# Kernel tuning notes

Hardware: AMD Instinct MI355X
Metric: run time of the kernel (lower is better)

The kernel has to match this reference:

```python
import jax, jax.numpy as jnp
import numpy as np

NUM_RADIAL = 6
HIDDEN = 128
OUT_EMB = 256
OUT_CH = 128
NUM_LAYERS = 3
E = 1600000
N_NODES = 50000


def setup_inputs() -> dict:
    key = jax.random.key(0)
    ks = jax.random.split(key, 16)
    inp = {
        "x": jax.random.normal(ks[0], (E, HIDDEN), dtype=jnp.float32),
        "rbf": jax.random.normal(ks[1], (E, NUM_RADIAL), dtype=jnp.float32),
        "idx_i": jax.random.randint(ks[2], (E,), 0, N_NODES, dtype=jnp.int32),
        "num_nodes": N_NODES,
        # torch nn.Linear weights are [out, in]
        "W_basis": jax.random.normal(ks[3], (HIDDEN, NUM_RADIAL), dtype=jnp.float32) * 0.3,
        "W_proj": jax.random.normal(ks[4], (OUT_EMB, HIDDEN), dtype=jnp.float32) * 0.08,
        "W_final": jax.random.normal(ks[5], (OUT_CH, OUT_EMB), dtype=jnp.float32) * 0.06,
    }
    for l in range(NUM_LAYERS):
        inp[f"W{l}"] = jax.random.normal(ks[6 + 2 * l], (OUT_EMB, OUT_EMB), dtype=jnp.float32) * 0.06
        inp[f"b{l}"] = jnp.zeros((OUT_EMB,), dtype=jnp.float32)
    return inp


def reference(x, rbf, idx_i, num_nodes, W_basis, W_proj, W_final, W0, b0, W1, b1, W2, b2):
    # basis_transformation: [E, num_radial] -> [E, hidden]
    basis = rbf @ W_basis.T
    # elementwise mul then edge->node scatter-sum
    msg = basis * x                                  # [E, hidden]
    agg = jax.ops.segment_sum(msg, idx_i, num_segments=num_nodes)  # [N, hidden]
    # output_projection (no bias)
    h = agg @ W_proj.T                                # [N, out_emb]
    for W, b in ((W0, b0), (W1, b1), (W2, b2)):
        h = jax.nn.silu(h @ W.T + b)
    return h @ W_final.T                              # [N, out_channels]
```

## Files before the change

### kernel.cpp

```cpp
#include <hip/hip_runtime.h>

typedef float f4 __attribute__((ext_vector_type(4)));
typedef float f2 __attribute__((ext_vector_type(2)));
typedef short bf16x8 __attribute__((ext_vector_type(8)));
typedef unsigned short u16x8 __attribute__((ext_vector_type(8)));
typedef unsigned short u16x4 __attribute__((ext_vector_type(4)));
typedef float f32x4 __attribute__((ext_vector_type(4)));

constexpr int HIDDEN     = 128;
constexpr int OUT_EMB    = 256;
constexpr int OUT_CH     = 128;
constexpr int NUM_RADIAL = 6;
constexpr int NBLK       = 64;

constexpr int OFF_Wp = 0;
constexpr int OFF_W0 = OFF_Wp + 256 * 128;
constexpr int OFF_W1 = OFF_W0 + 256 * 256;
constexpr int OFF_W2 = OFF_W1 + 256 * 256;
constexpr int OFF_Wf = OFF_W2 + 256 * 256;
constexpr int WTOT   = OFF_Wf + 128 * 256;

__device__ __forceinline__ unsigned short f2bf(float f) {
    unsigned int u = __float_as_uint(f);
    return (unsigned short)((u + 0x7FFFu + ((u >> 16) & 1u)) >> 16);
}
__device__ __forceinline__ float bf2f(unsigned short h) {
    return __uint_as_float(((unsigned int)h) << 16);
}

__global__ __launch_bounds__(256) void prep_kernel(
    const float* __restrict__ Wp, const float* __restrict__ W0,
    const float* __restrict__ W1, const float* __restrict__ W2,
    const float* __restrict__ Wf,
    unsigned short* __restrict__ whi, unsigned short* __restrict__ wlo,
    int* __restrict__ count, int N)
{
    const int i = blockIdx.x * 256 + threadIdx.x;
    if (i < N) count[i] = 0;
    if (i < WTOT) {
        const float* src; int off;
        if      (i < OFF_W0) { src = Wp; off = i - OFF_Wp; }
        else if (i < OFF_W1) { src = W0; off = i - OFF_W0; }
        else if (i < OFF_W2) { src = W1; off = i - OFF_W1; }
        else if (i < OFF_Wf) { src = W2; off = i - OFF_W2; }
        else                 { src = Wf; off = i - OFF_Wf; }
        float v = src[off];
        unsigned short h = f2bf(v);
        whi[i] = h;
        wlo[i] = f2bf(v - bf2f(h));
    }
}

__global__ __launch_bounds__(256) void hist_kernel(const int* __restrict__ idx,
                                                   int* __restrict__ count, long E)
{
    long i = (long)blockIdx.x * blockDim.x + threadIdx.x;
    if (i < E) atomicAdd(&count[idx[i]], 1);
}

__global__ __launch_bounds__(1024) void scan_kernel(const int* __restrict__ count,
                                                    int* __restrict__ start,
                                                    int* __restrict__ cursor, int N)
{
    __shared__ int part[1024];
    const int tid   = threadIdx.x;
    const int chunk = (N + 1023) / 1024;
    const int lo    = tid * chunk;
    const int hi    = min(lo + chunk, N);

    int s = 0;
    for (int i = lo; i < hi; ++i) s += count[i];
    part[tid] = s;
    __syncthreads();

    for (int off = 1; off < 1024; off <<= 1) {
        int v = part[tid];
        int u = (tid >= off) ? part[tid - off] : 0;
        __syncthreads();
        part[tid] = v + u;
        __syncthreads();
    }

    int run = (tid > 0) ? part[tid - 1] : 0;
    for (int i = lo; i < hi; ++i) {
        start[i]  = run;
        cursor[i] = run;
        run += count[i];
    }
    if (tid == 1023) start[N] = part[1023];
}

__global__ __launch_bounds__(256) void scatter_perm_kernel(const int* __restrict__ idx,
                                                           int* __restrict__ cursor,
                                                           int* __restrict__ perm, long E)
{
    long i = (long)blockIdx.x * blockDim.x + threadIdx.x;
    if (i < E) {
        int p = atomicAdd(&cursor[idx[i]], 1);
        perm[p] = (int)i;
    }
}

__device__ __forceinline__ void edge_accum(const float* __restrict__ x,
                                           const float* __restrict__ rbf,
                                           const float wb[4][NUM_RADIAL],
                                           int e, int l, f4& acc)
{
    const float* rp = rbf + (long)e * NUM_RADIAL;
    f2 r01 = *(const f2*)(rp);
    f2 r23 = *(const f2*)(rp + 2);
    f2 r45 = *(const f2*)(rp + 4);
    f4 xv  = *(const f4*)(x + (long)e * HIDDEN + 4 * l);
    float rb[NUM_RADIAL] = {r01[0], r01[1], r23[0], r23[1], r45[0], r45[1]};
#pragma unroll
    for (int c = 0; c < 4; ++c) {
        float b = 0.f;
#pragma unroll
        for (int r = 0; r < NUM_RADIAL; ++r) b = __builtin_fmaf(rb[r], wb[c][r], b);
        acc[c] = __builtin_fmaf(b, xv[c], acc[c]);
    }
}

__global__ __launch_bounds__(256) void gather_kernel(
    const float* __restrict__ x, const float* __restrict__ rbf,
    const float* __restrict__ Wb, const int* __restrict__ perm,
    const int* __restrict__ start, unsigned short* __restrict__ aggb, int N)
{
    const int lane = threadIdx.x & 63;
    const int half = lane >> 5;
    const int l    = lane & 31;
    const int wid  = threadIdx.x >> 6;
    const int node = blockIdx.x * 4 + wid;
    if (node >= N) return;

    float wb[4][NUM_RADIAL];
#pragma unroll
    for (int c = 0; c < 4; ++c)
#pragma unroll
        for (int r = 0; r < NUM_RADIAL; ++r)
            wb[c][r] = Wb[(4 * l + c) * NUM_RADIAL + r];

    const int j0 = start[node], j1 = start[node + 1];
    f4 acc = {0.f, 0.f, 0.f, 0.f};

    int j = j0 + half;
    for (; j + 2 < j1; j += 4) {
        const int ea = perm[j];
        const int eb = perm[j + 2];
        edge_accum(x, rbf, wb, ea, l, acc);
        edge_accum(x, rbf, wb, eb, l, acc);
    }
    if (j < j1) edge_accum(x, rbf, wb, perm[j], l, acc);

#pragma unroll
    for (int c = 0; c < 4; ++c) acc[c] += __shfl_xor(acc[c], 32);

    if (half == 0) {
        u16x4 o;
#pragma unroll
        for (int c = 0; c < 4; ++c) o[c] = f2bf(acc[c]);
        *(u16x4*)(aggb + (long)node * HIDDEN + 4 * l) = o;
    }
}

__device__ __forceinline__ int swz(int node, int col) {
    return (node * 256 + col) ^ ((node & 7) << 3);
}

template <int IN, int OUT, bool BIAS_ACT, bool LAST>
__device__ __forceinline__ void mfma_layer(
    const unsigned short* __restrict__ whi, const unsigned short* __restrict__ wlo,
    const float* __restrict__ bias,
    unsigned short* H, float* __restrict__ outp,
    int node0, int N, int w, int lane)
{
    const int lr = lane & 15;
    const int lg = lane >> 4;
    constexpr int NT = OUT / 64;
    const int wbase = w * (OUT / 4);

    f32x4 acc[4][NT];
#pragma unroll
    for (int nt = 0; nt < NT; ++nt) {
        float bb = 0.f;
        if constexpr (BIAS_ACT) bb = bias[wbase + nt * 16 + lr];
#pragma unroll
        for (int mt = 0; mt < 4; ++mt) {
            acc[mt][nt][0] = bb; acc[mt][nt][1] = bb;
            acc[mt][nt][2] = bb; acc[mt][nt][3] = bb;
        }
    }

    for (int ks = 0; ks < IN / 32; ++ks) {
        const int k0 = ks * 32 + lg * 8;
        bf16x8 ah[4];
#pragma unroll
        for (int mt = 0; mt < 4; ++mt) {
            const int node = mt * 16 + lr;
            ah[mt] = *(const bf16x8*)&H[swz(node, k0)];
        }
#pragma unroll
        for (int nt = 0; nt < NT; ++nt) {
            const long wrow = (long)(wbase + nt * 16 + lr) * IN + k0;
            bf16x8 bh = *(const bf16x8*)&whi[wrow];
            bf16x8 bl = *(const bf16x8*)&wlo[wrow];
#pragma unroll
            for (int mt = 0; mt < 4; ++mt) {
                acc[mt][nt] = __builtin_amdgcn_mfma_f32_16x16x32_bf16(ah[mt], bh, acc[mt][nt], 0, 0, 0);
                acc[mt][nt] = __builtin_amdgcn_mfma_f32_16x16x32_bf16(ah[mt], bl, acc[mt][nt], 0, 0, 0);
            }
        }
    }

    __syncthreads();

#pragma unroll
    for (int mt = 0; mt < 4; ++mt) {
#pragma unroll
        for (int nt = 0; nt < NT; ++nt) {
#pragma unroll
            for (int r = 0; r < 4; ++r) {
                float v = acc[mt][nt][r];
                if constexpr (BIAS_ACT) v = v / (1.f + __expf(-v));
                const int node = mt * 16 + lg * 4 + r;
                const int col  = wbase + nt * 16 + lr;
                if constexpr (LAST) {
                    if (node0 + node < N) outp[(long)(node0 + node) * OUT + col] = v;
                } else {
                    H[swz(node, col)] = f2bf(v);
                }
            }
        }
    }
    if constexpr (!LAST) __syncthreads();
}

__global__ __launch_bounds__(256, 3) void node_mlp_mfma_kernel(
    const unsigned short* __restrict__ aggb,
    const unsigned short* __restrict__ whi, const unsigned short* __restrict__ wlo,
    const float* __restrict__ b0, const float* __restrict__ b1,
    const float* __restrict__ b2,
    float* __restrict__ out, int N)
{
    __shared__ unsigned short H[NBLK * 256];

    const int tid   = threadIdx.x;
    const int w     = tid >> 6;
    const int lane  = tid & 63;
    const int node0 = blockIdx.x * NBLK;

#pragma unroll
    for (int i = 0; i < (NBLK * HIDDEN) / (256 * 8); ++i) {
        const int e    = (i * 256 + tid) * 8;
        const int node = e >> 7;
        const int col  = e & 127;
        u16x8 v = {0, 0, 0, 0, 0, 0, 0, 0};
        if (node0 + node < N) v = *(const u16x8*)(aggb + (long)(node0 + node) * HIDDEN + col);
        *(u16x8*)&H[swz(node, col)] = v;
    }
    __syncthreads();

    mfma_layer<HIDDEN,  OUT_EMB, false, false>(whi + OFF_Wp, wlo + OFF_Wp, nullptr, H, nullptr, node0, N, w, lane);
    mfma_layer<OUT_EMB, OUT_EMB, true,  false>(whi + OFF_W0, wlo + OFF_W0, b0,      H, nullptr, node0, N, w, lane);
    mfma_layer<OUT_EMB, OUT_EMB, true,  false>(whi + OFF_W1, wlo + OFF_W1, b1,      H, nullptr, node0, N, w, lane);
    mfma_layer<OUT_EMB, OUT_EMB, true,  false>(whi + OFF_W2, wlo + OFF_W2, b2,      H, nullptr, node0, N, w, lane);
    mfma_layer<OUT_EMB, OUT_CH,  false, true >(whi + OFF_Wf, wlo + OFF_Wf, nullptr, H, out,     node0, N, w, lane);
}

extern "C" void kernel_launch(void* const* d_in, const int* in_sizes, int n_in,
                              void* d_out, int out_size, void* d_ws, size_t ws_size,
                              hipStream_t stream)
{
    const float* x   = (const float*)d_in[0];
    const float* rbf = (const float*)d_in[1];
    const int*   idx = (const int*)d_in[2];
    const float* Wb  = (const float*)d_in[4];
    const float* Wp  = (const float*)d_in[5];
    const float* Wf  = (const float*)d_in[6];
    const float* W0  = (const float*)d_in[7];
    const float* b0  = (const float*)d_in[8];
    const float* W1  = (const float*)d_in[9];
    const float* b1  = (const float*)d_in[10];
    const float* W2  = (const float*)d_in[11];
    const float* b2  = (const float*)d_in[12];

    const long E = (long)in_sizes[0] / HIDDEN;
    const int  N = out_size / OUT_CH;

    unsigned short* aggb = (unsigned short*)d_ws;
    int* count  = (int*)(aggb + (long)N * HIDDEN);
    int* startp = count + N;
    int* cursor = startp + N + 1;
    int* perm   = cursor + N;
    uintptr_t p = (uintptr_t)(perm + E);
    p = (p + 15) & ~(uintptr_t)15;
    unsigned short* whi = (unsigned short*)p;
    unsigned short* wlo = whi + WTOT;

    const int pb = (max((int)WTOT, N) + 255) / 256;
    prep_kernel<<<pb, 256, 0, stream>>>(Wp, W0, W1, W2, Wf, whi, wlo, count, N);

    const int eb = (int)((E + 255) / 256);
    hist_kernel<<<eb, 256, 0, stream>>>(idx, count, E);
    scan_kernel<<<1, 1024, 0, stream>>>(count, startp, cursor, N);
    scatter_perm_kernel<<<eb, 256, 0, stream>>>(idx, cursor, perm, E);
    gather_kernel<<<(N + 3) / 4, 256, 0, stream>>>(x, rbf, Wb, perm, startp, aggb, N);

    node_mlp_mfma_kernel<<<(N + NBLK - 1) / NBLK, 256, 0, stream>>>(
        aggb, whi, wlo, b0, b1, b2, (float*)d_out, N);
}
```

Measured before the change: 719.2 us.

## Fuse edge gather into node MLP kernel and vectorize histogram/scatter

Removes the separate gather kernel and its bf16 aggregate buffer. Each MLP block now gathers its own 64 nodes, with each wave walking 16 nodes in turn, and writes the aggregated rows straight into shared memory before the MFMA layers. The histogram and permutation-scatter kernels also load four indices per thread with one vector load. This drops a kernel launch and a global round trip. The cost is far fewer concurrent waves for the latency-bound irregular gather, and the occupancy hint on the MLP kernel is gone.

```diff
diff --git a/kernel.cpp b/kernel.cpp
--- a/kernel.cpp
+++ b/kernel.cpp
@@ -2,6 +2,7 @@
 
 typedef float f4 __attribute__((ext_vector_type(4)));
 typedef float f2 __attribute__((ext_vector_type(2)));
+typedef int   i4 __attribute__((ext_vector_type(4)));
 typedef short bf16x8 __attribute__((ext_vector_type(8)));
 typedef unsigned short u16x8 __attribute__((ext_vector_type(8)));
 typedef unsigned short u16x4 __attribute__((ext_vector_type(4)));
@@ -54,8 +55,14 @@
 __global__ __launch_bounds__(256) void hist_kernel(const int* __restrict__ idx,
                                                    int* __restrict__ count, long E)
 {
-    long i = (long)blockIdx.x * blockDim.x + threadIdx.x;
-    if (i < E) atomicAdd(&count[idx[i]], 1);
+    long i = ((long)blockIdx.x * blockDim.x + threadIdx.x) * 4;
+    if (i + 3 < E) {
+        i4 v = *(const i4*)(idx + i);
+#pragma unroll
+        for (int k = 0; k < 4; ++k) atomicAdd(&count[v[k]], 1);
+    } else {
+        for (long t = i; t < E; ++t) atomicAdd(&count[idx[t]], 1);
+    }
 }
 
 __global__ __launch_bounds__(1024) void scan_kernel(const int* __restrict__ count,
@@ -94,11 +101,24 @@
                                                            int* __restrict__ cursor,
                                                            int* __restrict__ perm, long E)
 {
-    long i = (long)blockIdx.x * blockDim.x + threadIdx.x;
-    if (i < E) {
-        int p = atomicAdd(&cursor[idx[i]], 1);
-        perm[p] = (int)i;
-    }
+    long i = ((long)blockIdx.x * blockDim.x + threadIdx.x) * 4;
+    if (i + 3 < E) {
+        i4 v = *(const i4*)(idx + i);
+#pragma unroll
+        for (int k = 0; k < 4; ++k) {
+            int p = atomicAdd(&cursor[v[k]], 1);
+            perm[p] = (int)(i + k);
+        }
+    } else {
+        for (long t = i; t < E; ++t) {
+            int p = atomicAdd(&cursor[idx[t]], 1);
+            perm[p] = (int)t;
+        }
+    }
+}
+
+__device__ __forceinline__ int swz(int node, int col) {
+    return (node * 256 + col) ^ ((node & 7) << 3);
 }
 
 __device__ __forceinline__ void edge_accum(const float* __restrict__ x,
@@ -119,52 +139,6 @@
         for (int r = 0; r < NUM_RADIAL; ++r) b = __builtin_fmaf(rb[r], wb[c][r], b);
         acc[c] = __builtin_fmaf(b, xv[c], acc[c]);
     }
-}
-
-__global__ __launch_bounds__(256) void gather_kernel(
-    const float* __restrict__ x, const float* __restrict__ rbf,
-    const float* __restrict__ Wb, const int* __restrict__ perm,
-    const int* __restrict__ start, unsigned short* __restrict__ aggb, int N)
-{
-    const int lane = threadIdx.x & 63;
-    const int half = lane >> 5;
-    const int l    = lane & 31;
-    const int wid  = threadIdx.x >> 6;
-    const int node = blockIdx.x * 4 + wid;
-    if (node >= N) return;
-
-    float wb[4][NUM_RADIAL];
-#pragma unroll
-    for (int c = 0; c < 4; ++c)
-#pragma unroll
-        for (int r = 0; r < NUM_RADIAL; ++r)
-            wb[c][r] = Wb[(4 * l + c) * NUM_RADIAL + r];
-
-    const int j0 = start[node], j1 = start[node + 1];
-    f4 acc = {0.f, 0.f, 0.f, 0.f};
-
-    int j = j0 + half;
-    for (; j + 2 < j1; j += 4) {
-        const int ea = perm[j];
-        const int eb = perm[j + 2];
-        edge_accum(x, rbf, wb, ea, l, acc);
-        edge_accum(x, rbf, wb, eb, l, acc);
-    }
-    if (j < j1) edge_accum(x, rbf, wb, perm[j], l, acc);
-
-#pragma unroll
-    for (int c = 0; c < 4; ++c) acc[c] += __shfl_xor(acc[c], 32);
-
-    if (half == 0) {
-        u16x4 o;
-#pragma unroll
-        for (int c = 0; c < 4; ++c) o[c] = f2bf(acc[c]);
-        *(u16x4*)(aggb + (long)node * HIDDEN + 4 * l) = o;
-    }
-}
-
-__device__ __forceinline__ int swz(int node, int col) {
-    return (node * 256 + col) ^ ((node & 7) << 3);
 }
 
 template <int IN, int OUT, bool BIAS_ACT, bool LAST>
@@ -235,8 +209,10 @@
     if constexpr (!LAST) __syncthreads();
 }
 
-__global__ __launch_bounds__(256, 3) void node_mlp_mfma_kernel(
-    const unsigned short* __restrict__ aggb,
+__global__ __launch_bounds__(256) void fused_gather_mlp_kernel(
+    const float* __restrict__ x, const float* __restrict__ rbf,
+    const float* __restrict__ Wb,
+    const int* __restrict__ perm, const int* __restrict__ start,
     const unsigned short* __restrict__ whi, const unsigned short* __restrict__ wlo,
     const float* __restrict__ b0, const float* __restrict__ b1,
     const float* __restrict__ b2,
@@ -247,16 +223,43 @@
     const int tid   = threadIdx.x;
     const int w     = tid >> 6;
     const int lane  = tid & 63;
+    const int half  = lane >> 5;
+    const int l     = lane & 31;
     const int node0 = blockIdx.x * NBLK;
 
-#pragma unroll
-    for (int i = 0; i < (NBLK * HIDDEN) / (256 * 8); ++i) {
-        const int e    = (i * 256 + tid) * 8;
-        const int node = e >> 7;
-        const int col  = e & 127;
-        u16x8 v = {0, 0, 0, 0, 0, 0, 0, 0};
-        if (node0 + node < N) v = *(const u16x8*)(aggb + (long)(node0 + node) * HIDDEN + col);
-        *(u16x8*)&H[swz(node, col)] = v;
+    float wb[4][NUM_RADIAL];
+#pragma unroll
+    for (int c = 0; c < 4; ++c)
+#pragma unroll
+        for (int r = 0; r < NUM_RADIAL; ++r)
+            wb[c][r] = Wb[(4 * l + c) * NUM_RADIAL + r];
+
+    for (int nn = 0; nn < 16; ++nn) {
+        const int lrow = w * 16 + nn;
+        const int node = node0 + lrow;
+        f4 acc = {0.f, 0.f, 0.f, 0.f};
+
+        if (node < N) {
+            const int j0 = start[node], j1 = start[node + 1];
+            int j = j0 + half;
+            for (; j + 2 < j1; j += 4) {
+                const int ea = perm[j];
+                const int eb = perm[j + 2];
+                edge_accum(x, rbf, wb, ea, l, acc);
+                edge_accum(x, rbf, wb, eb, l, acc);
+            }
+            if (j < j1) edge_accum(x, rbf, wb, perm[j], l, acc);
+        }
+
+#pragma unroll
+        for (int c = 0; c < 4; ++c) acc[c] += __shfl_xor(acc[c], 32);
+
+        if (half == 0) {
+            u16x4 o;
+#pragma unroll
+            for (int c = 0; c < 4; ++c) o[c] = f2bf(acc[c]);
+            *(u16x4*)&H[swz(lrow, 4 * l)] = o;
+        }
     }
     __syncthreads();
 
@@ -287,8 +290,7 @@
     const long E = (long)in_sizes[0] / HIDDEN;
     const int  N = out_size / OUT_CH;
 
-    unsigned short* aggb = (unsigned short*)d_ws;
-    int* count  = (int*)(aggb + (long)N * HIDDEN);
+    int* count  = (int*)d_ws;
     int* startp = count + N;
     int* cursor = startp + N + 1;
     int* perm   = cursor + N;
@@ -300,12 +302,12 @@
     const int pb = (max((int)WTOT, N) + 255) / 256;
     prep_kernel<<<pb, 256, 0, stream>>>(Wp, W0, W1, W2, Wf, whi, wlo, count, N);
 
-    const int eb = (int)((E + 255) / 256);
+    const long Eq = (E + 3) / 4;
+    const int eb = (int)((Eq + 255) / 256);
     hist_kernel<<<eb, 256, 0, stream>>>(idx, count, E);
     scan_kernel<<<1, 1024, 0, stream>>>(count, startp, cursor, N);
     scatter_perm_kernel<<<eb, 256, 0, stream>>>(idx, cursor, perm, E);
-    gather_kernel<<<(N + 3) / 4, 256, 0, stream>>>(x, rbf, Wb, perm, startp, aggb, N);
-
-    node_mlp_mfma_kernel<<<(N + NBLK - 1) / NBLK, 256, 0, stream>>>(
-        aggb, whi, wlo, b0, b1, b2, (float*)d_out, N);
-}
+
+    fused_gather_mlp_kernel<<<(N + NBLK - 1) / NBLK, 256, 0, stream>>>(
+        x, rbf, Wb, perm, startp, whi, wlo, b0, b1, b2, (float*)d_out, N);
+}
```

Result: slower. 1.068 ms (+48.5%).

## Enlarge MLP node tile with 2x4 wave grid and vectorize histogram/scatter

Applied to the files above, without the earlier changes.

The node MLP kernel now processes 128 nodes per block with 512 threads arranged as 2 row-groups by 4 column-groups, so each weight fragment loaded from global memory feeds twice as many nodes. The histogram and permutation-scatter kernels load four indices per thread with a vector load, and the gather loop is unrolled to keep four edges in flight per half-wave. The larger LDS tile (64 KB) and higher launch bounds may cut occupancy or increase register pressure.

```diff
diff --git a/kernel.cpp b/kernel.cpp
--- a/kernel.cpp
+++ b/kernel.cpp
@@ -2,6 +2,7 @@
 
 typedef float f4 __attribute__((ext_vector_type(4)));
 typedef float f2 __attribute__((ext_vector_type(2)));
+typedef int   i4 __attribute__((ext_vector_type(4)));
 typedef short bf16x8 __attribute__((ext_vector_type(8)));
 typedef unsigned short u16x8 __attribute__((ext_vector_type(8)));
 typedef unsigned short u16x4 __attribute__((ext_vector_type(4)));
@@ -11,7 +12,7 @@
 constexpr int OUT_EMB    = 256;
 constexpr int OUT_CH     = 128;
 constexpr int NUM_RADIAL = 6;
-constexpr int NBLK       = 64;
+constexpr int NBLK       = 128;
 
 constexpr int OFF_Wp = 0;
 constexpr int OFF_W0 = OFF_Wp + 256 * 128;
@@ -54,8 +55,14 @@
 __global__ __launch_bounds__(256) void hist_kernel(const int* __restrict__ idx,
                                                    int* __restrict__ count, long E)
 {
-    long i = (long)blockIdx.x * blockDim.x + threadIdx.x;
-    if (i < E) atomicAdd(&count[idx[i]], 1);
+    long i = ((long)blockIdx.x * blockDim.x + threadIdx.x) * 4;
+    if (i + 3 < E) {
+        i4 v = *(const i4*)(idx + i);
+#pragma unroll
+        for (int k = 0; k < 4; ++k) atomicAdd(&count[v[k]], 1);
+    } else {
+        for (long t = i; t < E; ++t) atomicAdd(&count[idx[t]], 1);
+    }
 }
 
 __global__ __launch_bounds__(1024) void scan_kernel(const int* __restrict__ count,
@@ -94,10 +101,19 @@
                                                            int* __restrict__ cursor,
                                                            int* __restrict__ perm, long E)
 {
-    long i = (long)blockIdx.x * blockDim.x + threadIdx.x;
-    if (i < E) {
-        int p = atomicAdd(&cursor[idx[i]], 1);
-        perm[p] = (int)i;
+    long i = ((long)blockIdx.x * blockDim.x + threadIdx.x) * 4;
+    if (i + 3 < E) {
+        i4 v = *(const i4*)(idx + i);
+#pragma unroll
+        for (int k = 0; k < 4; ++k) {
+            int p = atomicAdd(&cursor[v[k]], 1);
+            perm[p] = (int)(i + k);
+        }
+    } else {
+        for (long t = i; t < E; ++t) {
+            int p = atomicAdd(&cursor[idx[t]], 1);
+            perm[p] = (int)t;
+        }
     }
 }
 
@@ -144,13 +160,17 @@
     f4 acc = {0.f, 0.f, 0.f, 0.f};
 
     int j = j0 + half;
-    for (; j + 2 < j1; j += 4) {
-        const int ea = perm[j];
-        const int eb = perm[j + 2];
-        edge_accum(x, rbf, wb, ea, l, acc);
-        edge_accum(x, rbf, wb, eb, l, acc);
-    }
-    if (j < j1) edge_accum(x, rbf, wb, perm[j], l, acc);
+    for (; j + 6 < j1; j += 8) {
+        const int e0 = perm[j];
+        const int e1 = perm[j + 2];
+        const int e2 = perm[j + 4];
+        const int e3 = perm[j + 6];
+        edge_accum(x, rbf, wb, e0, l, acc);
+        edge_accum(x, rbf, wb, e1, l, acc);
+        edge_accum(x, rbf, wb, e2, l, acc);
+        edge_accum(x, rbf, wb, e3, l, acc);
+    }
+    for (; j < j1; j += 2) edge_accum(x, rbf, wb, perm[j], l, acc);
 
 #pragma unroll
     for (int c = 0; c < 4; ++c) acc[c] += __shfl_xor(acc[c], 32);
@@ -172,12 +192,13 @@
     const unsigned short* __restrict__ whi, const unsigned short* __restrict__ wlo,
     const float* __restrict__ bias,
     unsigned short* H, float* __restrict__ outp,
-    int node0, int N, int w, int lane)
+    int node0, int N, int wm, int wn, int lane)
 {
     const int lr = lane & 15;
     const int lg = lane >> 4;
     constexpr int NT = OUT / 64;
-    const int wbase = w * (OUT / 4);
+    const int wbase = wn * (OUT / 4);
+    const int mrow0 = wm * 64;
 
     f32x4 acc[4][NT];
 #pragma unroll
@@ -195,10 +216,8 @@
         const int k0 = ks * 32 + lg * 8;
         bf16x8 ah[4];
 #pragma unroll
-        for (int mt = 0; mt < 4; ++mt) {
-            const int node = mt * 16 + lr;
-            ah[mt] = *(const bf16x8*)&H[swz(node, k0)];
-        }
+        for (int mt = 0; mt < 4; ++mt)
+            ah[mt] = *(const bf16x8*)&H[swz(mrow0 + mt * 16 + lr, k0)];
 #pragma unroll
         for (int nt = 0; nt < NT; ++nt) {
             const long wrow = (long)(wbase + nt * 16 + lr) * IN + k0;
@@ -222,7 +241,7 @@
             for (int r = 0; r < 4; ++r) {
                 float v = acc[mt][nt][r];
                 if constexpr (BIAS_ACT) v = v / (1.f + __expf(-v));
-                const int node = mt * 16 + lg * 4 + r;
+                const int node = mrow0 + mt * 16 + lg * 4 + r;
                 const int col  = wbase + nt * 16 + lr;
                 if constexpr (LAST) {
                     if (node0 + node < N) outp[(long)(node0 + node) * OUT + col] = v;
@@ -235,7 +254,7 @@
     if constexpr (!LAST) __syncthreads();
 }
 
-__global__ __launch_bounds__(256, 3) void node_mlp_mfma_kernel(
+__global__ __launch_bounds__(512, 4) void node_mlp_mfma_kernel(
     const unsigned short* __restrict__ aggb,
     const unsigned short* __restrict__ whi, const unsigned short* __restrict__ wlo,
     const float* __restrict__ b0, const float* __restrict__ b1,
@@ -247,11 +266,13 @@
     const int tid   = threadIdx.x;
     const int w     = tid >> 6;
     const int lane  = tid & 63;
+    const int wm    = w >> 2;
+    const int wn    = w & 3;
     const int node0 = blockIdx.x * NBLK;
 
 #pragma unroll
-    for (int i = 0; i < (NBLK * HIDDEN) / (256 * 8); ++i) {
-        const int e    = (i * 256 + tid) * 8;
+    for (int i = 0; i < (NBLK * HIDDEN) / (512 * 8); ++i) {
+        const int e    = (i * 512 + tid) * 8;
         const int node = e >> 7;
         const int col  = e & 127;
         u16x8 v = {0, 0, 0, 0, 0, 0, 0, 0};
@@ -260,11 +281,11 @@
     }
     __syncthreads();
 
-    mfma_layer<HIDDEN,  OUT_EMB, false, false>(whi + OFF_Wp, wlo + OFF_Wp, nullptr, H, nullptr, node0, N, w, lane);
-    mfma_layer<OUT_EMB, OUT_EMB, true,  false>(whi + OFF_W0, wlo + OFF_W0, b0,      H, nullptr, node0, N, w, lane);
-    mfma_layer<OUT_EMB, OUT_EMB, true,  false>(whi + OFF_W1, wlo + OFF_W1, b1,      H, nullptr, node0, N, w, lane);
-    mfma_layer<OUT_EMB, OUT_EMB, true,  false>(whi + OFF_W2, wlo + OFF_W2, b2,      H, nullptr, node0, N, w, lane);
-    mfma_layer<OUT_EMB, OUT_CH,  false, true >(whi + OFF_Wf, wlo + OFF_Wf, nullptr, H, out,     node0, N, w, lane);
+    mfma_layer<HIDDEN,  OUT_EMB, false, false>(whi + OFF_Wp, wlo + OFF_Wp, nullptr, H, nullptr, node0, N, wm, wn, lane);
+    mfma_layer<OUT_EMB, OUT_EMB, true,  false>(whi + OFF_W0, wlo + OFF_W0, b0,      H, nullptr, node0, N, wm, wn, lane);
+    mfma_layer<OUT_EMB, OUT_EMB, true,  false>(whi + OFF_W1, wlo + OFF_W1, b1,      H, nullptr, node0, N, wm, wn, lane);
+    mfma_layer<OUT_EMB, OUT_EMB, true,  false>(whi + OFF_W2, wlo + OFF_W2, b2,      H, nullptr, node0, N, wm, wn, lane);
+    mfma_layer<OUT_EMB, OUT_CH,  false, true >(whi + OFF_Wf, wlo + OFF_Wf, nullptr, H, out,     node0, N, wm, wn, lane);
 }
 
 extern "C" void kernel_launch(void* const* d_in, const int* in_sizes, int n_in,
@@ -300,12 +321,13 @@
     const int pb = (max((int)WTOT, N) + 255) / 256;
     prep_kernel<<<pb, 256, 0, stream>>>(Wp, W0, W1, W2, Wf, whi, wlo, count, N);
 
-    const int eb = (int)((E + 255) / 256);
+    const long Eq = (E + 3) / 4;
+    const int eb = (int)((Eq + 255) / 256);
     hist_kernel<<<eb, 256, 0, stream>>>(idx, count, E);
     scan_kernel<<<1, 1024, 0, stream>>>(count, startp, cursor, N);
     scatter_perm_kernel<<<eb, 256, 0, stream>>>(idx, cursor, perm, E);
     gather_kernel<<<(N + 3) / 4, 256, 0, stream>>>(x, rbf, Wb, perm, startp, aggb, N);
 
-    node_mlp_mfma_kernel<<<(N + NBLK - 1) / NBLK, 256, 0, stream>>>(
+    node_mlp_mfma_kernel<<<(N + NBLK - 1) / NBLK, 512, 0, stream>>>(
         aggb, whi, wlo, b0, b1, b2, (float*)d_out, N);
 }
```

Result: faster. 702.6 us (-2.3%).
